# Optimization experiments

Measured on AMD Instinct MI355X. Metric: run time of the kernel, lower is better.

## Reference

```python
import jax, jax.numpy as jnp
import numpy as np

WIN = 2048          # n_fft == win_length in the original module
HOP = 256           # hop_length from __init__
F0_MIN = 50.0
AC_FFT = 4096       # >= 2*1025-1, for linear (non-circular) autocorrelation


def _stft_magnitude(audio):
    """Replicates torch.stft(center=True, reflect pad, periodic Hann). -> (1025, T)"""
    n = jnp.arange(WIN, dtype=audio.dtype)
    window = 0.5 * (1.0 - jnp.cos(2.0 * jnp.pi * n / WIN))  # periodic Hann
    padded = jnp.pad(audio, (WIN // 2, WIN // 2), mode='reflect')
    T = audio.shape[0] // HOP + 1
    idx = jnp.arange(T)[:, None] * HOP + jnp.arange(WIN)[None, :]
    frames = padded[idx] * window                       # (T, 2048)
    spec = jnp.fft.rfft(frames, axis=-1)                # (T, 1025)
    return jnp.abs(spec).T                              # (1025, T)


def _autocorrelation(mag):
    """autocorr[lag, t] = sum_k mag[k, t] * mag[k+lag, t] for lag in 1..F//2-1.
    Computed via Wiener-Khinchin (FFT) instead of the O(F^2) Python loops."""
    F = mag.shape[0]  # 1025
    ps = jnp.abs(jnp.fft.rfft(mag, n=AC_FFT, axis=0)) ** 2   # power spectrum
    r = jnp.fft.irfft(ps, n=AC_FFT, axis=0)[:F]              # (F, T) linear autocorr
    lag = jnp.arange(F)
    valid = (lag >= 1) & (lag < F // 2)                      # original fills only lags 1..F//2-1
    return r * valid[:, None].astype(mag.dtype)


def _autocorr_to_f0(ac):
    """Original sets f0[t] = f0_min if any interior local max exists in ac[1:, t]."""
    s = ac[1:, :]                                            # drop lag 0 (signal[1:])
    peaks = (s[1:-1, :] > s[:-2, :]) & (s[1:-1, :] > s[2:, :])
    has_peak = jnp.any(peaks, axis=0)
    return jnp.where(has_peak, jnp.asarray(F0_MIN, ac.dtype), jnp.asarray(0.0, ac.dtype))


def _median_smoothing(f0, kernel_size=5):
    pad = kernel_size // 2
    p = jnp.pad(f0, (pad, pad), mode='edge')                 # replicate padding
    T = f0.shape[0]
    windows = jnp.stack([p[i:i + T] for i in range(kernel_size)], axis=-1)  # (T, 5)
    return jnp.median(windows, axis=-1)


def setup_inputs() -> dict:
    key = jax.random.key(0)
    audio = jax.random.normal(key, (2097152,), dtype=jnp.float32)
    return {"audio": audio}


def reference(audio) -> jnp.ndarray:
    mag = _stft_magnitude(audio)       # (1025, T)
    ac = _autocorrelation(mag)         # (1025, T)
    f0 = _autocorr_to_f0(ac)           # (T,)
    return _median_smoothing(f0, 5)    # (T,)
```

## Files before the change

kernel.cpp:

```cpp
#include <hip/hip_runtime.h>
#include <math.h>

#define HOP 256
#define PI2F 6.28318530717958647692f
#define PADZ(i) ((i) + ((i) >> 4))

#define C16 0.92387953251128675613f
#define S16 0.38268343236508977173f
#define RH  0.70710678118654752440f

#define FENCE() do { asm volatile("s_waitcnt lgkmcnt(0)" ::: "memory"); \
                     __builtin_amdgcn_sched_barrier(0); } while (0)

__global__ __launch_bounds__(256) void precompute(float* __restrict__ win,
                                                  float2* __restrict__ gtw,
                                                  float2* __restrict__ guw) {
  const int i = blockIdx.x * blockDim.x + threadIdx.x;
  if (i < 2048) win[i] = 0.5f * (1.0f - cosf(PI2F * (float)i / 2048.0f));
  if (i < 512) {
    float s, c; sincosf(-PI2F * (float)i / 1024.0f, &s, &c);
    gtw[i] = make_float2(c, s);
  }
  if (i < 513) {
    float s, c; sincosf(-PI2F * (float)i / 2048.0f, &s, &c);
    guw[i] = make_float2(c, s);
  }
}

__device__ __forceinline__ float2 cadd(float2 a, float2 b){ return make_float2(a.x+b.x, a.y+b.y); }
__device__ __forceinline__ float2 csub(float2 a, float2 b){ return make_float2(a.x-b.x, a.y-b.y); }
__device__ __forceinline__ float2 cmul(float2 a, float2 b){
  return make_float2(fmaf(a.x, b.x, -a.y*b.y), fmaf(a.x, b.y, a.y*b.x));
}
__device__ __forceinline__ float2 mul_mj(float2 v){ return make_float2(v.y, -v.x); }
__device__ __forceinline__ float2 mul_pj(float2 v){ return make_float2(-v.y, v.x); }
__device__ __forceinline__ float2 tw1f(float2 v){ return make_float2(fmaf(C16,v.x, S16*v.y), fmaf(C16,v.y,-S16*v.x)); }
__device__ __forceinline__ float2 tw2f(float2 v){ return make_float2(RH*(v.x+v.y), RH*(v.y-v.x)); }
__device__ __forceinline__ float2 tw3f(float2 v){ return make_float2(fmaf(S16,v.x, C16*v.y), fmaf(S16,v.y,-C16*v.x)); }
__device__ __forceinline__ float2 tw4f(float2 v){ return make_float2(v.y, -v.x); }
__device__ __forceinline__ float2 tw6f(float2 v){ return make_float2(RH*(v.y-v.x), -RH*(v.x+v.y)); }
__device__ __forceinline__ float2 tw9f(float2 v){ return make_float2(fmaf(-C16,v.x,-S16*v.y), fmaf(S16,v.x,-C16*v.y)); }

__device__ __forceinline__ void dft4(float2 a, float2 b, float2 c, float2 d,
                                     float2& o0, float2& o1, float2& o2, float2& o3) {
  const float2 t0 = cadd(a, c), t1 = csub(a, c);
  const float2 t2 = cadd(b, d), t3 = csub(b, d);
  o0 = cadd(t0, t2);
  o2 = csub(t0, t2);
  o1 = cadd(t1, mul_mj(t3));
  o3 = cadd(t1, mul_pj(t3));
}

__device__ __forceinline__ void dft16(float2 v[16]) {
  float2 A0[4], A1[4], A2[4], A3[4];
  dft4(v[0], v[4], v[ 8], v[12], A0[0], A0[1], A0[2], A0[3]);
  dft4(v[1], v[5], v[ 9], v[13], A1[0], A1[1], A1[2], A1[3]);
  dft4(v[2], v[6], v[10], v[14], A2[0], A2[1], A2[2], A2[3]);
  dft4(v[3], v[7], v[11], v[15], A3[0], A3[1], A3[2], A3[3]);
  dft4(A0[0],       A1[0],        A2[0],        A3[0],       v[0], v[4], v[ 8], v[12]);
  dft4(A0[1], tw1f(A1[1]), tw2f(A2[1]), tw3f(A3[1]), v[1], v[5], v[ 9], v[13]);
  dft4(A0[2], tw2f(A1[2]), tw4f(A2[2]), tw6f(A3[2]), v[2], v[6], v[10], v[14]);
  dft4(A0[3], tw3f(A1[3]), tw6f(A2[3]), tw9f(A3[3]), v[3], v[7], v[11], v[15]);
}

__device__ __forceinline__ void wave_fft1024(float2* __restrict__ zw, float2 v[16],
                                             const int l, const float2* __restrict__ gtw) {
  dft16(v);
  {
    const float2 w1 = gtw[l];
    float2 w = w1;
    #pragma unroll
    for (int s = 1; s < 16; ++s) { v[s] = cmul(v[s], w); w = cmul(w, w1); }
  }
  #pragma unroll
  for (int s = 0; s < 16; ++s) zw[65 * s + l] = v[s];
  FENCE();
  const int sp = l >> 2, n0 = l & 3;
  #pragma unroll
  for (int r = 0; r < 16; ++r) v[r] = zw[65 * sp + n0 + 4 * r];
  dft16(v);
  {
    const float2 wb = gtw[n0 << 4];
    float2 w = wb;
    #pragma unroll
    for (int u = 1; u < 16; ++u) { v[u] = cmul(v[u], w); w = cmul(w, wb); }
  }
  #pragma unroll
  for (int u = 0; u < 16; ++u) zw[65 * sp + 4 * u + n0] = v[u];
  FENCE();
  #pragma unroll
  for (int b = 0; b < 4; ++b)
    #pragma unroll
    for (int m0 = 0; m0 < 4; ++m0)
      v[4 * b + m0] = zw[65 * sp + 16 * n0 + 4 * b + m0];
  FENCE();
  #pragma unroll
  for (int b = 0; b < 4; ++b) {
    float2 o0, o1, o2, o3;
    dft4(v[4*b+0], v[4*b+1], v[4*b+2], v[4*b+3], o0, o1, o2, o3);
    const int kb = 64 * n0 + 16 * b + sp;
    zw[PADZ(kb      )] = o0;
    zw[PADZ(kb + 256)] = o1;
    zw[PADZ(kb + 512)] = o2;
    zw[PADZ(kb + 768)] = o3;
  }
  FENCE();
}

template<int MODE>
__device__ __forceinline__ void untangle(const float2* __restrict__ zw,
                                         float* __restrict__ mp, const int l,
                                         const float2* __restrict__ guw) {
  #pragma unroll
  for (int c = 0; c < 8; ++c) {
    const int k = l + 64 * c;
    const int m = (1024 - k) & 1023;
    const float2 Zk = zw[PADZ(k)];
    const float2 Zm = zw[PADZ(m)];
    const float Er = 0.5f * (Zk.x + Zm.x), Ei = 0.5f * (Zk.y - Zm.y);
    const float Or = 0.5f * (Zk.y + Zm.y), Oi = 0.5f * (Zm.x - Zk.x);
    const float2 w = guw[k];
    const float wOr = w.x * Or - w.y * Oi;
    const float wOi = w.x * Oi + w.y * Or;
    if (MODE == 2) {
      if (k >= 1) mp[k] = Er + wOr;
    } else {
      const float Xr = Er + wOr, Xi =  Ei + wOi;
      const float Yr = Er - wOr, Yi = -Ei + wOi;
      if (MODE == 0) {
        mp[k]        = sqrtf(Xr * Xr + Xi * Xi);
        mp[1024 - k] = sqrtf(Yr * Yr + Yi * Yi);
      } else {
        mp[k]        = Xr * Xr + Xi * Xi;
        mp[1024 - k] = Yr * Yr + Yi * Yi;
      }
    }
  }
  if (l == 0) {
    const float2 Z5 = zw[PADZ(512)];
    if (MODE == 0)      mp[512] = sqrtf(Z5.x * Z5.x + Z5.y * Z5.y);
    else if (MODE == 1) mp[512] = Z5.x * Z5.x + Z5.y * Z5.y;
    else                mp[512] = 0.0f;
  }
}

__global__ __launch_bounds__(256, 3) void pitch_main(const float* __restrict__ audio,
    int N, int T, float* __restrict__ f0,
    const float* __restrict__ gwin, const float2* __restrict__ gtw,
    const float2* __restrict__ guw) {
  __shared__ float2 zbuf[4][1088];
  __shared__ float  mpbuf[4][1028];
  const int wv = threadIdx.x >> 6;
  const int l  = threadIdx.x & 63;
  const int frame = blockIdx.x * 4 + wv;
  if (frame >= T) return;
  float2* zw = zbuf[wv];
  float*  mp = mpbuf[wv];
  float2  v[16];

  const int base = frame * HOP - 1024;
  if (base >= 0 && base + 2048 <= N) {
    const float2* au2 = (const float2*)(audio + base);
    const float2* wi2 = (const float2*)gwin;
    #pragma unroll
    for (int j = 0; j < 16; ++j) {
      const float2 a = au2[l + 64 * j];
      const float2 w = wi2[l + 64 * j];
      v[j] = make_float2(a.x * w.x, a.y * w.y);
    }
  } else {
    #pragma unroll
    for (int j = 0; j < 16; ++j) {
      const int i2 = 2 * (l + 64 * j);
      int j0 = base + i2, j1 = base + i2 + 1;
      j0 = (j0 < 0) ? -j0 : j0; j0 = (j0 >= N) ? (2 * N - 2 - j0) : j0;
      j1 = (j1 < 0) ? -j1 : j1; j1 = (j1 >= N) ? (2 * N - 2 - j1) : j1;
      v[j] = make_float2(audio[j0] * gwin[i2], audio[j1] * gwin[i2 + 1]);
    }
  }
  wave_fft1024(zw, v, l, gtw);
  untangle<0>(zw, mp, l, guw);
  FENCE();

  {
    const float2* mp2 = (const float2*)mp;
    #pragma unroll
    for (int j = 0; j < 8; ++j) v[j] = mp2[l + 64 * j];
    const float mv = mp[1024];
    v[8] = make_float2((l == 0) ? mv : 0.0f, 0.0f);
    #pragma unroll
    for (int j = 9; j < 16; ++j) v[j] = make_float2(0.0f, 0.0f);
  }
  wave_fft1024(zw, v, l, gtw);
  untangle<1>(zw, mp, l, guw);
  FENCE();

  {
    const float2* mp2 = (const float2*)mp;
    #pragma unroll
    for (int j = 0; j < 8; ++j) v[j] = mp2[l + 64 * j];
    #pragma unroll
    for (int j = 8; j < 16; ++j) {
      const int m2 = 1024 - (l + 64 * j);
      v[j] = make_float2(mp2[m2].x, mp2[m2 - 1].y);
    }
  }
  wave_fft1024(zw, v, l, gtw);
  untangle<2>(zw, mp, l, guw);
  FENCE();

  int cond = 0;
  #pragma unroll
  for (int c = 0; c < 8; ++c) {
    const int k = l + 64 * c;
    if (k >= 2) {
      const float c0 = mp[k];
      if (c0 > mp[k - 1] && c0 > mp[k + 1]) cond = 1;
    }
  }
  const int has = __any(cond);
  if (l == 0) f0[frame] = has ? 50.0f : 0.0f;
}

__global__ __launch_bounds__(256) void median5_kernel(const float* __restrict__ f0,
                                                      float* __restrict__ out, int T) {
  const int t = blockIdx.x * blockDim.x + threadIdx.x;
  if (t >= T) return;
  float v[5];
  #pragma unroll
  for (int m = 0; m < 5; ++m) {
    int idx = t + m - 2;
    idx = idx < 0 ? 0 : (idx > T - 1 ? T - 1 : idx);
    v[m] = f0[idx];
  }
  #define SW(a,b) { float lo = fminf(v[a], v[b]); float hi = fmaxf(v[a], v[b]); v[a] = lo; v[b] = hi; }
  SW(0,1); SW(3,4); SW(2,4); SW(2,3); SW(1,4); SW(0,3); SW(0,2); SW(1,3); SW(1,2);
  #undef SW
  out[t] = v[2];
}

extern "C" void kernel_launch(void* const* d_in, const int* in_sizes, int n_in,
                              void* d_out, int out_size, void* d_ws, size_t ws_size,
                              hipStream_t stream) {
  const float* audio = (const float*)d_in[0];
  const int n = in_sizes[0];
  const int T = n / HOP + 1;

  float* ws   = (float*)d_ws;
  float* f0   = ws;
  float* win  = ws + 8200;
  float2* gtw = (float2*)(ws + 10248);
  float2* guw = (float2*)(ws + 11272);

  precompute<<<8, 256, 0, stream>>>(win, gtw, guw);
  pitch_main<<<(T + 3) / 4, 256, 0, stream>>>(audio, n, T, f0, win, gtw, guw);
  median5_kernel<<<(T + 255) / 256, 256, 0, stream>>>(f0, (float*)d_out, T);
}
```

Baseline: 121.4 us.

## Fuse median into main kernel, table twiddles, drop mp buffer for occupancy

Three separate ideas are combined. The recursive twiddle multiplication in both FFT stages is replaced by lookups into a precomputed per-lane twiddle table. The separate magnitude scratch buffer is removed by writing magnitudes into the real part of the FFT buffer, which cuts LDS use and raises the occupancy hint from 3 to 4 blocks per CU. The median5 kernel launch is removed: the last block to finish, found with an atomic counter, runs the median smoothing. The cost is that this tail work runs serially on a single block, plus extra global loads for the twiddle table and strided LDS reads for the packed inputs.

Measured after the change: 298.1 us. 146% more time.

```diff
diff --git a/kernel.cpp b/kernel.cpp
--- a/kernel.cpp
+++ b/kernel.cpp
@@ -13,18 +13,21 @@
                      __builtin_amdgcn_sched_barrier(0); } while (0)
 
 __global__ __launch_bounds__(256) void precompute(float* __restrict__ win,
-                                                  float2* __restrict__ gtw,
-                                                  float2* __restrict__ guw) {
+                                                  float2* __restrict__ gtwA,
+                                                  float2* __restrict__ guw,
+                                                  unsigned* __restrict__ cnt) {
   const int i = blockIdx.x * blockDim.x + threadIdx.x;
   if (i < 2048) win[i] = 0.5f * (1.0f - cosf(PI2F * (float)i / 2048.0f));
-  if (i < 512) {
-    float s, c; sincosf(-PI2F * (float)i / 1024.0f, &s, &c);
-    gtw[i] = make_float2(c, s);
+  if (i < 1024) {
+    const int s2 = i >> 6, l = i & 63;
+    float s, c; sincosf(-PI2F * (float)(l * s2) / 1024.0f, &s, &c);
+    gtwA[i] = make_float2(c, s);
   }
   if (i < 513) {
     float s, c; sincosf(-PI2F * (float)i / 2048.0f, &s, &c);
     guw[i] = make_float2(c, s);
   }
+  if (i == 0) *cnt = 0u;
 }
 
 __device__ __forceinline__ float2 cadd(float2 a, float2 b){ return make_float2(a.x+b.x, a.y+b.y); }
@@ -64,14 +67,11 @@
 }
 
 __device__ __forceinline__ void wave_fft1024(float2* __restrict__ zw, float2 v[16],
-                                             const int l, const float2* __restrict__ gtw) {
+                                             const int l,
+                                             const float2* __restrict__ gtwA) {
   dft16(v);
-  {
-    const float2 w1 = gtw[l];
-    float2 w = w1;
-    #pragma unroll
-    for (int s = 1; s < 16; ++s) { v[s] = cmul(v[s], w); w = cmul(w, w1); }
-  }
+  #pragma unroll
+  for (int s = 1; s < 16; ++s) v[s] = cmul(v[s], gtwA[(s << 6) + l]);
   #pragma unroll
   for (int s = 0; s < 16; ++s) zw[65 * s + l] = v[s];
   FENCE();
@@ -79,12 +79,8 @@
   #pragma unroll
   for (int r = 0; r < 16; ++r) v[r] = zw[65 * sp + n0 + 4 * r];
   dft16(v);
-  {
-    const float2 wb = gtw[n0 << 4];
-    float2 w = wb;
-    #pragma unroll
-    for (int u = 1; u < 16; ++u) { v[u] = cmul(v[u], w); w = cmul(w, wb); }
-  }
+  #pragma unroll
+  for (int u = 1; u < 16; ++u) v[u] = cmul(v[u], gtwA[(u << 6) + (n0 << 4)]);
   #pragma unroll
   for (int u = 0; u < 16; ++u) zw[65 * sp + 4 * u + n0] = v[u];
   FENCE();
@@ -108,8 +104,8 @@
 }
 
 template<int MODE>
-__device__ __forceinline__ void untangle(const float2* __restrict__ zw,
-                                         float* __restrict__ mp, const int l,
+__device__ __forceinline__ void untangle(float2* __restrict__ zw,
+                                         const int l,
                                          const float2* __restrict__ guw) {
   #pragma unroll
   for (int c = 0; c < 8; ++c) {
@@ -123,120 +119,139 @@
     const float wOr = w.x * Or - w.y * Oi;
     const float wOi = w.x * Oi + w.y * Or;
     if (MODE == 2) {
-      if (k >= 1) mp[k] = Er + wOr;
+      if (k >= 1) zw[PADZ(k)].x = Er + wOr;
     } else {
       const float Xr = Er + wOr, Xi =  Ei + wOi;
       const float Yr = Er - wOr, Yi = -Ei + wOi;
       if (MODE == 0) {
-        mp[k]        = sqrtf(Xr * Xr + Xi * Xi);
-        mp[1024 - k] = sqrtf(Yr * Yr + Yi * Yi);
+        zw[PADZ(k)].x        = sqrtf(Xr * Xr + Xi * Xi);
+        zw[PADZ(1024 - k)].x = sqrtf(Yr * Yr + Yi * Yi);
       } else {
-        mp[k]        = Xr * Xr + Xi * Xi;
-        mp[1024 - k] = Yr * Yr + Yi * Yi;
+        zw[PADZ(k)].x        = Xr * Xr + Xi * Xi;
+        zw[PADZ(1024 - k)].x = Yr * Yr + Yi * Yi;
       }
     }
   }
   if (l == 0) {
     const float2 Z5 = zw[PADZ(512)];
-    if (MODE == 0)      mp[512] = sqrtf(Z5.x * Z5.x + Z5.y * Z5.y);
-    else if (MODE == 1) mp[512] = Z5.x * Z5.x + Z5.y * Z5.y;
-    else                mp[512] = 0.0f;
-  }
-}
-
-__global__ __launch_bounds__(256, 3) void pitch_main(const float* __restrict__ audio,
-    int N, int T, float* __restrict__ f0,
-    const float* __restrict__ gwin, const float2* __restrict__ gtw,
-    const float2* __restrict__ guw) {
-  __shared__ float2 zbuf[4][1088];
-  __shared__ float  mpbuf[4][1028];
+    if (MODE == 0)      zw[PADZ(512)].x = sqrtf(Z5.x * Z5.x + Z5.y * Z5.y);
+    else if (MODE == 1) zw[PADZ(512)].x = Z5.x * Z5.x + Z5.y * Z5.y;
+    else                zw[PADZ(512)].x = 0.0f;
+  }
+}
+
+__global__ __launch_bounds__(256, 4) void pitch_main(const float* __restrict__ audio,
+    int N, int T, float* __restrict__ f0, float* __restrict__ out,
+    const float* __restrict__ gwin, const float2* __restrict__ gtwA,
+    const float2* __restrict__ guw, unsigned* __restrict__ cnt) {
+  __shared__ float2 zbuf[4][1092];
+  __shared__ int lastFlag;
   const int wv = threadIdx.x >> 6;
   const int l  = threadIdx.x & 63;
   const int frame = blockIdx.x * 4 + wv;
-  if (frame >= T) return;
-  float2* zw = zbuf[wv];
-  float*  mp = mpbuf[wv];
-  float2  v[16];
-
-  const int base = frame * HOP - 1024;
-  if (base >= 0 && base + 2048 <= N) {
-    const float2* au2 = (const float2*)(audio + base);
-    const float2* wi2 = (const float2*)gwin;
-    #pragma unroll
-    for (int j = 0; j < 16; ++j) {
-      const float2 a = au2[l + 64 * j];
-      const float2 w = wi2[l + 64 * j];
-      v[j] = make_float2(a.x * w.x, a.y * w.y);
-    }
-  } else {
-    #pragma unroll
-    for (int j = 0; j < 16; ++j) {
-      const int i2 = 2 * (l + 64 * j);
-      int j0 = base + i2, j1 = base + i2 + 1;
-      j0 = (j0 < 0) ? -j0 : j0; j0 = (j0 >= N) ? (2 * N - 2 - j0) : j0;
-      j1 = (j1 < 0) ? -j1 : j1; j1 = (j1 >= N) ? (2 * N - 2 - j1) : j1;
-      v[j] = make_float2(audio[j0] * gwin[i2], audio[j1] * gwin[i2 + 1]);
-    }
-  }
-  wave_fft1024(zw, v, l, gtw);
-  untangle<0>(zw, mp, l, guw);
-  FENCE();
-
-  {
-    const float2* mp2 = (const float2*)mp;
-    #pragma unroll
-    for (int j = 0; j < 8; ++j) v[j] = mp2[l + 64 * j];
-    const float mv = mp[1024];
-    v[8] = make_float2((l == 0) ? mv : 0.0f, 0.0f);
-    #pragma unroll
-    for (int j = 9; j < 16; ++j) v[j] = make_float2(0.0f, 0.0f);
-  }
-  wave_fft1024(zw, v, l, gtw);
-  untangle<1>(zw, mp, l, guw);
-  FENCE();
-
-  {
-    const float2* mp2 = (const float2*)mp;
-    #pragma unroll
-    for (int j = 0; j < 8; ++j) v[j] = mp2[l + 64 * j];
+  const bool active = frame < T;
+
+  if (active) {
+    float2* zw = zbuf[wv];
+    float2  v[16];
+
+    const int base = frame * HOP - 1024;
+    if (base >= 0 && base + 2048 <= N) {
+      const float2* au2 = (const float2*)(audio + base);
+      const float2* wi2 = (const float2*)gwin;
+      #pragma unroll
+      for (int j = 0; j < 16; ++j) {
+        const float2 a = au2[l + 64 * j];
+        const float2 w = wi2[l + 64 * j];
+        v[j] = make_float2(a.x * w.x, a.y * w.y);
+      }
+    } else {
+      #pragma unroll
+      for (int j = 0; j < 16; ++j) {
+        const int i2 = 2 * (l + 64 * j);
+        int j0 = base + i2, j1 = base + i2 + 1;
+        j0 = (j0 < 0) ? -j0 : j0; j0 = (j0 >= N) ? (2 * N - 2 - j0) : j0;
+        j1 = (j1 < 0) ? -j1 : j1; j1 = (j1 >= N) ? (2 * N - 2 - j1) : j1;
+        v[j] = make_float2(audio[j0] * gwin[i2], audio[j1] * gwin[i2 + 1]);
+      }
+    }
+    wave_fft1024(zw, v, l, gtwA);
+    untangle<0>(zw, l, guw);
+    FENCE();
+
+    #pragma unroll
+    for (int j = 0; j < 8; ++j) {
+      const int i = l + 64 * j;
+      v[j] = make_float2(zw[PADZ(2 * i)].x, zw[PADZ(2 * i + 1)].x);
+    }
+    {
+      const float mv = zw[1088].x;
+      v[8] = make_float2((l == 0) ? mv : 0.0f, 0.0f);
+      #pragma unroll
+      for (int j = 9; j < 16; ++j) v[j] = make_float2(0.0f, 0.0f);
+    }
+    wave_fft1024(zw, v, l, gtwA);
+    untangle<1>(zw, l, guw);
+    FENCE();
+
+    #pragma unroll
+    for (int j = 0; j < 8; ++j) {
+      const int i = l + 64 * j;
+      v[j] = make_float2(zw[PADZ(2 * i)].x, zw[PADZ(2 * i + 1)].x);
+    }
     #pragma unroll
     for (int j = 8; j < 16; ++j) {
-      const int m2 = 1024 - (l + 64 * j);
-      v[j] = make_float2(mp2[m2].x, mp2[m2 - 1].y);
-    }
-  }
-  wave_fft1024(zw, v, l, gtw);
-  untangle<2>(zw, mp, l, guw);
-  FENCE();
-
-  int cond = 0;
-  #pragma unroll
-  for (int c = 0; c < 8; ++c) {
-    const int k = l + 64 * c;
-    if (k >= 2) {
-      const float c0 = mp[k];
-      if (c0 > mp[k - 1] && c0 > mp[k + 1]) cond = 1;
-    }
-  }
-  const int has = __any(cond);
-  if (l == 0) f0[frame] = has ? 50.0f : 0.0f;
-}
-
-__global__ __launch_bounds__(256) void median5_kernel(const float* __restrict__ f0,
-                                                      float* __restrict__ out, int T) {
-  const int t = blockIdx.x * blockDim.x + threadIdx.x;
-  if (t >= T) return;
-  float v[5];
-  #pragma unroll
-  for (int m = 0; m < 5; ++m) {
-    int idx = t + m - 2;
-    idx = idx < 0 ? 0 : (idx > T - 1 ? T - 1 : idx);
-    v[m] = f0[idx];
-  }
-  #define SW(a,b) { float lo = fminf(v[a], v[b]); float hi = fmaxf(v[a], v[b]); v[a] = lo; v[b] = hi; }
-  SW(0,1); SW(3,4); SW(2,4); SW(2,3); SW(1,4); SW(0,3); SW(0,2); SW(1,3); SW(1,2);
-  #undef SW
-  out[t] = v[2];
+      const int i  = l + 64 * j;
+      const int e0 = 2048 - 2 * i;
+      v[j] = make_float2(zw[PADZ(e0)].x, zw[PADZ(e0 - 1)].x);
+    }
+    wave_fft1024(zw, v, l, gtwA);
+    untangle<2>(zw, l, guw);
+    FENCE();
+
+    int cond = 0;
+    #pragma unroll
+    for (int c = 0; c < 8; ++c) {
+      const int k = l + 64 * c;
+      if (k >= 2) {
+        const float c0 = zw[PADZ(k)].x;
+        if (c0 > zw[PADZ(k - 1)].x && c0 > zw[PADZ(k + 1)].x) cond = 1;
+      }
+    }
+    const int has = __any(cond);
+    if (l == 0)
+      __hip_atomic_store(&f0[frame], has ? 50.0f : 0.0f,
+                         __ATOMIC_RELAXED, __HIP_MEMORY_SCOPE_AGENT);
+  }
+
+  __syncthreads();
+  if (threadIdx.x == 0) {
+    const unsigned old = __hip_atomic_fetch_add(cnt, 1u, __ATOMIC_ACQ_REL,
+                                                __HIP_MEMORY_SCOPE_AGENT);
+    lastFlag = (old == (unsigned)(gridDim.x - 1)) ? 1 : 0;
+  }
+  __syncthreads();
+  if (lastFlag) {
+    float* fsh = (float*)&zbuf[0][0];
+    for (int t0 = threadIdx.x; t0 < T; t0 += 256)
+      fsh[t0 + 2] = __hip_atomic_load(&f0[t0], __ATOMIC_RELAXED,
+                                      __HIP_MEMORY_SCOPE_AGENT);
+    __syncthreads();
+    if (threadIdx.x == 0) {
+      fsh[0] = fsh[1] = fsh[2];
+      fsh[T + 2] = fsh[T + 3] = fsh[T + 1];
+    }
+    __syncthreads();
+    for (int t0 = threadIdx.x; t0 < T; t0 += 256) {
+      float v0 = fsh[t0], v1 = fsh[t0 + 1], v2 = fsh[t0 + 2],
+            v3 = fsh[t0 + 3], v4 = fsh[t0 + 4];
+      #define SW(a,b) { const float lo = fminf(a, b); const float hi = fmaxf(a, b); a = lo; b = hi; }
+      SW(v0,v1); SW(v3,v4); SW(v2,v4); SW(v2,v3); SW(v1,v4);
+      SW(v0,v3); SW(v0,v2); SW(v1,v3); SW(v1,v2);
+      #undef SW
+      out[t0] = v2;
+    }
+  }
 }
 
 extern "C" void kernel_launch(void* const* d_in, const int* in_sizes, int n_in,
@@ -246,13 +261,14 @@
   const int n = in_sizes[0];
   const int T = n / HOP + 1;
 
-  float* ws   = (float*)d_ws;
-  float* f0   = ws;
-  float* win  = ws + 8200;
-  float2* gtw = (float2*)(ws + 10248);
-  float2* guw = (float2*)(ws + 11272);
-
-  precompute<<<8, 256, 0, stream>>>(win, gtw, guw);
-  pitch_main<<<(T + 3) / 4, 256, 0, stream>>>(audio, n, T, f0, win, gtw, guw);
-  median5_kernel<<<(T + 255) / 256, 256, 0, stream>>>(f0, (float*)d_out, T);
-}
+  float* ws    = (float*)d_ws;
+  float* f0    = ws;
+  float* win   = ws + 8200;
+  float2* gtwA = (float2*)(ws + 10248);
+  float2* guw  = (float2*)(ws + 12296);
+  unsigned* cnt = (unsigned*)(ws + 13322);
+
+  precompute<<<8, 256, 0, stream>>>(win, gtwA, guw, cnt);
+  pitch_main<<<(T + 3) / 4, 256, 0, stream>>>(audio, n, T, f0, (float*)d_out,
+                                              win, gtwA, guw, cnt);
+}
```
